# Kernel optimization log

Hardware: AMD Instinct MI355X
Metric: run time of the kernel (lower is better)

## Reference

```python
import jax, jax.numpy as jnp
import numpy as np

# ---- straight-through binary quantizers (custom VJP matches torch autograd.Functions) ----
@jax.custom_vjp
def bq(x):
    return jnp.sign(x)
def _bq_fwd(x):
    return jnp.sign(x), x
def _bq_bwd(x, g):
    return (g * ((x > -1.0) & (x < 1.0)).astype(g.dtype),)
bq.defvjp(_bq_fwd, _bq_bwd)

@jax.custom_vjp
def bq_quad(x):
    return jnp.sign(x)
def _bqq_fwd(x):
    return jnp.sign(x), x
def _bqq_bwd(x, g):
    return (jnp.maximum(2.0 - jnp.abs(2.0 * x), 0.0) * g,)
bq_quad.defvjp(_bqq_fwd, _bqq_bwd)

def bilinear(x, W, s, b):
    # BiLinear: row-centered sign weights scaled by learned per-row factor, sign activations
    Wc = W - jnp.mean(W, axis=-1, keepdims=True)
    Wb = s * bq(Wc)                      # (out, in)
    return bq(x) @ Wb.T + b

def selective_scan(u, delta, A, Bs, Cs, D, delta_bias):
    # u, delta: (B,K,Dn,L); A: (K,Dn,N); Bs,Cs: (B,K,N,L); D, delta_bias: (K,Dn)
    Bn, K, Dn, L = u.shape
    N = A.shape[-1]
    delta = jax.nn.softplus(delta + delta_bias[None, :, :, None])
    def step(h, inp):
        ut, dt, Bt, Ct = inp             # (B,K,Dn),(B,K,Dn),(B,K,N),(B,K,N)
        dA = jnp.exp(dt[..., None] * A[None])
        h = dA * h + (dt * ut)[..., None] * Bt[:, :, None, :]
        y = jnp.einsum('bkdn,bkn->bkd', h, Ct)
        return h, y
    h0 = jnp.zeros((Bn, K, Dn, N), u.dtype)
    _, ys = jax.lax.scan(step, h0,
                         (u.transpose(3, 0, 1, 2), delta.transpose(3, 0, 1, 2),
                          Bs.transpose(3, 0, 1, 2), Cs.transpose(3, 0, 1, 2)))
    y = ys.transpose(1, 2, 3, 0)         # (B,K,Dn,L)
    return y + D[None, :, :, None] * u

def _forward(x, W_in, b_in, s_in, move0_b, conv_W, conv_b, rp_b0, prelu_a, rp_b1,
             Wl, bl, sl, Wd, bd, sd, dt_bias, A_logs, Ds, ln_w, ln_b, W_out, b_out, s_out):
    Bn, H, Wi, dm = x.shape
    Dn = conv_W.shape[0]
    K = 4
    N = A_logs.shape[1]
    R = Wd.shape[2]
    L = H * Wi
    xz = bilinear(x, W_in, s_in, b_in)                  # (B,H,W,2*Dn)
    xp, z = jnp.split(xz, 2, axis=-1)
    xc = xp.transpose(0, 3, 1, 2)                       # (B,Dn,H,W)
    # BConv2d: move0 bias -> sign (quad STE) -> binary conv -> RPReLU -> residual
    t = bq_quad(xc + move0_b[None, :, None, None])
    sc = jax.lax.stop_gradient(jnp.mean(jnp.abs(conv_W), axis=(1, 2, 3), keepdims=True))
    cw = jnp.clip(conv_W, -1.0, 1.0)
    Wb = jax.lax.stop_gradient(sc * jnp.sign(conv_W) - cw) + cw
    t = jax.lax.conv_general_dilated(t, Wb, (1, 1), [(1, 1), (1, 1)],
                                     dimension_numbers=('NCHW', 'OIHW', 'NCHW'))
    t = t + conv_b[None, :, None, None]
    t = t + rp_b0[None, :, None, None]
    t = jnp.where(t >= 0, t, prelu_a[None, :, None, None] * t)
    t = t + rp_b1[None, :, None, None] + xc
    xconv = jax.nn.silu(t)
    # 4-direction scan inputs
    x_flat = xconv.reshape(Bn, Dn, L)
    x_tr = xconv.transpose(0, 1, 3, 2).reshape(Bn, Dn, L)
    x_hwwh = jnp.stack([x_flat, x_tr], axis=1)
    xs = jnp.concatenate([x_hwwh, jnp.flip(x_hwwh, axis=-1)], axis=1)   # (B,K,Dn,L)
    # NOTE: torch does .view(B,L,-1) on contiguous (B,Dn,L) slices = raw reshape (not transpose)
    xin = xs.reshape(Bn, K, L, Dn)
    x_dbl = jax.vmap(bilinear, in_axes=(1, 0, 0, 0), out_axes=1)(xin, Wl, sl, bl)  # (B,K,L,R+2N)
    x_dbl = x_dbl.transpose(0, 1, 3, 2)                                 # (B,K,R+2N,L)
    dts_r, Bs, Cs = jnp.split(x_dbl, [R, R + N], axis=2)
    dts_in = dts_r.reshape(Bn, K, L, R)  # raw reshape, matches torch .view
    dts = jax.vmap(bilinear, in_axes=(1, 0, 0, 0), out_axes=1)(dts_in, Wd, sd, bd)  # (B,K,L,Dn)
    dts = dts.transpose(0, 1, 3, 2)                                     # (B,K,Dn,L)
    A = -jnp.exp(A_logs).reshape(K, Dn, N)
    out_y = selective_scan(xs, dts, A, Bs, Cs, Ds.reshape(K, Dn), dt_bias.reshape(K, Dn))
    inv_y = jnp.flip(out_y[:, 2:4], axis=-1)
    wh_y = out_y[:, 1].reshape(Bn, Dn, Wi, H).transpose(0, 1, 3, 2).reshape(Bn, Dn, L)
    invwh_y = inv_y[:, 1].reshape(Bn, Dn, Wi, H).transpose(0, 1, 3, 2).reshape(Bn, Dn, L)
    y = out_y[:, 0] + inv_y[:, 0] + wh_y + invwh_y                      # (B,Dn,L)
    y = y.transpose(0, 2, 1).reshape(Bn, H, Wi, Dn)
    mu = jnp.mean(y, axis=-1, keepdims=True)
    var = jnp.var(y, axis=-1, keepdims=True)
    y = (y - mu) / jnp.sqrt(var + 1e-5) * ln_w + ln_b                   # LayerNorm eps=1e-5
    y = y * jax.nn.silu(z)
    return bilinear(y, W_out, s_out, b_out)

def setup_inputs():
    key = jax.random.key(0)
    ks = jax.random.split(key, 12)
    B, H, Wi, dm = 4, 64, 64, 96
    Dn, N, R, K = 192, 16, 6, 4
    u = lambda k, sh, a: jax.random.uniform(k, sh, jnp.float32, -a, a)
    x = jax.random.normal(ks[0], (B, H, Wi, dm), jnp.float32)
    W_in = u(ks[1], (2 * Dn, dm), 0.015)
    b_in = u(ks[2], (2 * Dn,), 0.01)
    s_in = jnp.mean(jnp.abs(W_in), axis=1, keepdims=True)
    move0_b = jnp.zeros((Dn,), jnp.float32)
    conv_W = 0.05 * jax.random.normal(ks[3], (Dn, Dn, 3, 3), jnp.float32)
    conv_b = u(ks[4], (Dn,), 0.01)
    rp_b0 = jnp.zeros((Dn,), jnp.float32)
    prelu_a = 0.25 * jnp.ones((Dn,), jnp.float32)
    rp_b1 = jnp.zeros((Dn,), jnp.float32)
    Wl = u(ks[5], (K, R + 2 * N, Dn), 0.015)
    bl = u(ks[6], (K, R + 2 * N), 0.01)
    sl = jnp.mean(jnp.abs(Wl), axis=2, keepdims=True)
    std = R ** -0.5
    Wd = u(ks[7], (K, Dn, R), std)
    bd = u(ks[8], (K, Dn), 0.01)
    sd = jnp.mean(jnp.abs(Wd), axis=2, keepdims=True)
    dt = jnp.exp(jax.random.uniform(ks[9], (K * Dn,), jnp.float32)
                 * (np.log(0.1) - np.log(0.001)) + np.log(0.001))
    dt = jnp.clip(dt, 1e-4, None)
    dt_bias = dt + jnp.log(-jnp.expm1(-dt))
    A_logs = jnp.tile(jnp.log(jnp.arange(1, N + 1, dtype=jnp.float32))[None, :], (K * Dn, 1))
    Ds = jnp.ones((K * Dn,), jnp.float32)
    ln_w = jnp.ones((Dn,), jnp.float32)
    ln_b = jnp.zeros((Dn,), jnp.float32)
    W_out = u(ks[10], (dm, Dn), 0.015)
    b_out = u(ks[11], (dm,), 0.01)
    s_out = jnp.mean(jnp.abs(W_out), axis=1, keepdims=True)
    return dict(x=x, W_in=W_in, b_in=b_in, s_in=s_in, move0_b=move0_b, conv_W=conv_W,
                conv_b=conv_b, rp_b0=rp_b0, prelu_a=prelu_a, rp_b1=rp_b1, Wl=Wl, bl=bl,
                sl=sl, Wd=Wd, bd=bd, sd=sd, dt_bias=dt_bias, A_logs=A_logs, Ds=Ds,
                ln_w=ln_w, ln_b=ln_b, W_out=W_out, b_out=b_out, s_out=s_out)

def reference(x, W_in, b_in, s_in, move0_b, conv_W, conv_b, rp_b0, prelu_a, rp_b1,
              Wl, bl, sl, Wd, bd, sd, dt_bias, A_logs, Ds, ln_w, ln_b, W_out, b_out, s_out):
    return _forward(x, W_in, b_in, s_in, move0_b, conv_W, conv_b, rp_b0, prelu_a, rp_b1,
                    Wl, bl, sl, Wd, bd, sd, dt_bias, A_logs, Ds, ln_w, ln_b, W_out, b_out, s_out)
```

## Files before the change

### kernel.cpp

```cpp
#include <hip/hip_runtime.h>
#include <math.h>
#include <stdint.h>

#define BB 4
#define HH 64
#define WW2 64
#define DM 96
#define DN 192
#define KK 4
#define NN 16
#define RR 6
#define LL 4096
#define RN 38

#define LOG2E 1.4426950408889634f
#define LN2   0.6931471805599453f

#define OFF_WDB      0
#define OFF_WCS      4608
#define OFF_WAUX     15360
#define OFF_WSC      16896
#define OFF_WBIB     17088
#define OFF_WOUTB    18240
#define OFF_WLBB     18816
#define OFF_XBP      19728
#define OFF_PXS      19728
#define OFF_SSUM     19728
#define OFF_YB       19728
#define OFF_XC       412992
#define OFF_ZS       3558720
#define OFF_XCONV    6704448
#define OFF_XS       9850176
#define OFF_XDBL     22433088
#define OFF_HEND     OFF_XCONV

#define PLANE 4356

__device__ __forceinline__ float fsign(float v) {
  return (v > 0.f) ? 1.f : ((v < 0.f) ? -1.f : 0.f);
}
__device__ __forceinline__ float softplusf(float v) {
  return fmaxf(v, 0.f) + LN2 * log2f(1.f + exp2f(-fabsf(v) * LOG2E));
}
__device__ __forceinline__ float siluf(float v) {
  return v / (1.f + expf(-v));
}
__device__ __forceinline__ float waveAllSum(float s) {
  #pragma unroll
  for (int off = 32; off; off >>= 1) s += __shfl_xor(s, off, 64);
  return s;
}

__global__ __launch_bounds__(64) void k_prep(
    const float* __restrict__ W_in, const float* __restrict__ s_in,
    const float* __restrict__ W_out, const float* __restrict__ s_out,
    const float* __restrict__ Wl, const float* __restrict__ sl,
    const float* __restrict__ Wd, const float* __restrict__ sd,
    const float* __restrict__ convW, float* __restrict__ ws) {
  int r = blockIdx.x, lane = threadIdx.x;
  if (r < 384) {
    const float* row = W_in + r * DM;
    float s = 0.f;
    for (int c = lane; c < DM; c += 64) s += row[c];
    s = waveAllSum(s);
    float mean = s / (float)DM;
    if (lane < 3) {
      uint32_t wv = 0;
      #pragma unroll
      for (int i = 0; i < 32; ++i) wv |= (row[lane * 32 + i] - mean > 0.f ? 1u : 0u) << i;
      ((uint32_t*)(ws + OFF_WBIB))[r * 3 + lane] = wv;
    }
  } else if (r < 480) {
    int m = r - 384;
    const float* row = W_out + m * DN;
    float s = 0.f;
    for (int c = lane; c < DN; c += 64) s += row[c];
    s = waveAllSum(s);
    float mean = s / (float)DN;
    if (lane < 6) {
      uint32_t wv = 0;
      #pragma unroll
      for (int i = 0; i < 32; ++i) wv |= (row[lane * 32 + i] - mean > 0.f ? 1u : 0u) << i;
      ((uint32_t*)(ws + OFF_WOUTB))[m * 6 + lane] = wv;
    }
  } else if (r < 632) {
    int idx = r - 480;
    const float* row = Wl + idx * DN;
    float s = 0.f;
    for (int c = lane; c < DN; c += 64) s += row[c];
    s = waveAllSum(s);
    float mean = s / (float)DN;
    if (lane < 6) {
      uint32_t wv = 0;
      #pragma unroll
      for (int i = 0; i < 32; ++i) wv |= (row[lane * 32 + i] - mean > 0.f ? 1u : 0u) << i;
      ((uint32_t*)(ws + OFF_WLBB))[idx * 6 + lane] = wv;
    }
  } else if (r < 1400) {
    int idx = r - 632;
    const float* row = Wd + idx * RR;
    float s = (lane < RR) ? row[lane] : 0.f;
    s = waveAllSum(s);
    float mean = s / (float)RR;
    unsigned long long mb = __ballot((lane < RR) && (row[lane] - mean > 0.f));
    if (lane == 0) {
      ((uint32_t*)(ws + OFF_WDB))[idx] = (uint32_t)mb & 0x3Fu;
      (ws + OFF_WDB)[768 + idx] = sd[idx];
    }
  } else {
    int o = r - 1400;
    const float* row = convW + o * 1728;
    float s = 0.f;
    for (int j = lane; j < 1728; j += 64) s += fabsf(row[j]);
    s = waveAllSum(s);
    float sc = s / 1728.f;
    uint32_t* wb = (uint32_t*)(ws + OFF_WCS);
    int* aux = (int*)(ws + OFF_WAUX);
    float* scf = ws + OFF_WSC;
    uint32_t word = 0;
    if (lane < 54) {
      int cw = lane / 9, tap = lane % 9;
      #pragma unroll
      for (int i = 0; i < 32; ++i)
        word |= (row[(cw * 32 + i) * 9 + tap] > 0.f ? 1u : 0u) << i;
      wb[o * 56 + lane] = word;
    } else if (lane < 56) {
      wb[o * 56 + lane] = 0u;
    }
    int pc = (lane < 54) ? 2 * (int)__popc(word) - 32 : 0;
    int tapid = lane % 9;
    int wst = 0;
    #pragma unroll
    for (int cw = 0; cw < 6; ++cw) wst += __shfl(pc, cw * 9 + tapid, 64);
    int w_t[9];
    #pragma unroll
    for (int t9 = 0; t9 < 9; ++t9) w_t[t9] = __shfl(wst, t9, 64);
    if (lane == 0) {
      aux[o * 8 + 0] = w_t[0] + w_t[3] + w_t[6];
      aux[o * 8 + 1] = w_t[2] + w_t[5] + w_t[8];
      aux[o * 8 + 2] = w_t[0] + w_t[1] + w_t[2];
      aux[o * 8 + 3] = w_t[6] + w_t[7] + w_t[8];
      aux[o * 8 + 4] = w_t[0];
      aux[o * 8 + 5] = w_t[2];
      aux[o * 8 + 6] = w_t[6];
      aux[o * 8 + 7] = w_t[8];
      scf[o] = sc;
    }
  }
}

__global__ __launch_bounds__(384) void k_bilin_in(
    const float* __restrict__ x, const float* __restrict__ b_in,
    const float* __restrict__ s_in, const float* __restrict__ ws,
    float* __restrict__ xc, float* __restrict__ zs) {
  __shared__ uint32_t spx[16 * 3];
  __shared__ float sxz[384 * 17];
  int p0 = blockIdx.x * 16;
  if (threadIdx.x < 48) {
    int pix = threadIdx.x / 3, wd = threadIdx.x % 3;
    const float* base = x + (size_t)(p0 + pix) * DM + wd * 32;
    uint32_t wv = 0;
    #pragma unroll
    for (int i = 0; i < 32; ++i) wv |= (base[i] > 0.f ? 1u : 0u) << i;
    spx[pix * 3 + wd] = wv;
  }
  __syncthreads();
  int o = threadIdx.x;
  uint32_t w0, w1, w2;
  {
    const uint32_t* wb = (const uint32_t*)(ws + OFF_WBIB) + o * 3;
    w0 = wb[0]; w1 = wb[1]; w2 = wb[2];
  }
  float bias = b_in[o], sc = s_in[o];
  #pragma unroll
  for (int pix = 0; pix < 16; ++pix) {
    int P = (int)__popc(spx[pix * 3 + 0] ^ w0) + (int)__popc(spx[pix * 3 + 1] ^ w1) +
            (int)__popc(spx[pix * 3 + 2] ^ w2);
    sxz[o * 17 + pix] = bias + sc * (float)(DM - 2 * P);
  }
  __syncthreads();
  int b = p0 >> 12, l0 = p0 & 4095;
  for (int f = threadIdx.x; f < DN * 16; f += 384) {
    int od = f >> 4, pix = f & 15;
    xc[((size_t)(b * DN + od)) * LL + l0 + pix] = sxz[od * 17 + pix];
  }
  for (int f = threadIdx.x; f < DN * 16; f += 384) {
    int pix = f / DN, oz = f - pix * DN;
    zs[(size_t)(p0 + pix) * DN + oz] = siluf(sxz[(DN + oz) * 17 + pix]);
  }
}

__global__ __launch_bounds__(256) void k_pack(
    const float* __restrict__ xc, const float* __restrict__ move0,
    uint32_t* __restrict__ xb) {
  int t = blockIdx.x * 256 + threadIdx.x;
  int w2 = t & 31;
  int h = (t >> 5) & 63;
  int g = t >> 11;
  int cw = g % 6, b = g / 6;
  const float* xp = xc + ((size_t)(b * DN + cw * 32)) * LL + h * 64 + w2 * 2;
  uint32_t w0 = 0, w1 = 0;
  #pragma unroll
  for (int i = 0; i < 32; ++i) {
    float m = move0[cw * 32 + i];
    float2 v = *(const float2*)(xp + (size_t)i * LL);
    w0 |= (v.x + m > 0.f ? 1u : 0u) << i;
    w1 |= (v.y + m > 0.f ? 1u : 0u) << i;
  }
  uint32_t* plane = xb + (size_t)(b * 6 + cw) * PLANE;
  plane[(h + 1) * 66 + 1 + w2 * 2] = w0;
  plane[(h + 1) * 66 + 2 + w2 * 2] = w1;
}

__global__ __launch_bounds__(256) void k_conv(
    const uint32_t* __restrict__ xb, const float* __restrict__ xc,
    const uint32_t* __restrict__ wbits, const int* __restrict__ aux,
    const float* __restrict__ scf, const float* __restrict__ conv_b,
    const float* __restrict__ rp_b0, const float* __restrict__ prelu_a,
    const float* __restrict__ rp_b1, float* __restrict__ xconv) {
  int og = blockIdx.x & 3;
  int stripe = (blockIdx.x >> 2) & 15;
  int b = blockIdx.x >> 6;
  int w = threadIdx.x & 63, r = threadIdx.x >> 6;
  int h = stripe * 4 + r;

  __shared__ uint32_t swb[48 * 56];
  __shared__ int saux[48 * 8];
  __shared__ float sconst[48 * 4];
  for (int i = threadIdx.x; i < 48 * 56; i += 256) swb[i] = wbits[og * (48 * 56) + i];
  for (int i = threadIdx.x; i < 48 * 8; i += 256) saux[i] = aux[og * (48 * 8) + i];
  if (threadIdx.x < 48) {
    int o = og * 48 + threadIdx.x;
    sconst[threadIdx.x * 4 + 0] = scf[o];
    sconst[threadIdx.x * 4 + 1] = conv_b[o] + rp_b0[o];
    sconst[threadIdx.x * 4 + 2] = prelu_a[o];
    sconst[threadIdx.x * 4 + 3] = rp_b1[o];
  }

  uint32_t xw[6][9];
  const uint32_t* xpb = xb + (size_t)b * 6 * PLANE;
  #pragma unroll
  for (int cw = 0; cw < 6; ++cw) {
    const uint32_t* plane = xpb + cw * PLANE + (h + 1) * 66 + (w + 1);
    #pragma unroll
    for (int dy = 0; dy < 3; ++dy) {
      #pragma unroll
      for (int dx = 0; dx < 3; ++dx)
        xw[cw][dy * 3 + dx] = plane[(dy - 1) * 66 + (dx - 1)];
    }
  }
  bool isL = (w == 0), isR = (w == 63);
  bool isT = (h == 0), isB = (h == 63);
  const float* xcp = xc + ((size_t)(b * DN + og * 48)) * LL + h * 64 + w;
  float* xop = xconv + ((size_t)(b * DN + og * 48)) * LL + h * 64 + w;
  __syncthreads();

  #pragma unroll 1
  for (int oc = 0; oc < 48; ++oc) {
    const uint32_t* wp = &swb[oc * 56];
    int P = 0;
    #pragma unroll
    for (int cw = 0; cw < 6; ++cw) {
      int pp = 0;
      #pragma unroll
      for (int t = 0; t < 9; ++t) pp += (int)__popc(wp[cw * 9 + t] ^ xw[cw][t]);
      P += pp;
    }
    int corr = isL ? saux[oc * 8 + 0] : (isR ? saux[oc * 8 + 1] : 0);
    if (isT) {
      corr += saux[oc * 8 + 2];
      if (isL) corr -= saux[oc * 8 + 4];
      if (isR) corr -= saux[oc * 8 + 5];
    }
    if (isB) {
      corr += saux[oc * 8 + 3];
      if (isL) corr -= saux[oc * 8 + 6];
      if (isR) corr -= saux[oc * 8 + 7];
    }
    float acc = sconst[oc * 4 + 0] * (float)(1728 - 2 * P + corr);
    float t = acc + sconst[oc * 4 + 1];
    t = (t >= 0.f) ? t : sconst[oc * 4 + 2] * t;
    t += sconst[oc * 4 + 3] + *xcp;
    *xop = siluf(t);
    xcp += LL; xop += LL;
  }
}

__global__ __launch_bounds__(256) void k_build_xs(const float* __restrict__ xconv,
                                                  float* __restrict__ xs,
                                                  uint32_t* __restrict__ pxs) {
  __shared__ float tile[64][65];
  int bd = blockIdx.x;
  int b = bd / DN, d = bd % DN;
  const float* img = xconv + (size_t)bd * LL;
  for (int i = threadIdx.x; i < LL; i += 256)
    tile[i >> 6][i & 63] = img[i];
  __syncthreads();
  int lane = threadIdx.x & 63;
  #pragma unroll
  for (int k = 0; k < 4; ++k) {
    size_t base = ((size_t)((b * KK + k) * DN + d)) * LL;
    for (int j = threadIdx.x; j < LL; j += 256) {
      float v;
      if (k == 0)      v = tile[j >> 6][j & 63];
      else if (k == 1) v = tile[j & 63][j >> 6];
      else if (k == 2) { int t2 = 4095 - j; v = tile[t2 >> 6][t2 & 63]; }
      else             { int t2 = 4095 - j; v = tile[t2 & 63][t2 >> 6]; }
      xs[base + j] = v;
      unsigned long long m = __ballot(v > 0.f);
      if (lane == 0)       pxs[(base + j) >> 5] = (uint32_t)m;
      else if (lane == 32) pxs[(base + j) >> 5] = (uint32_t)(m >> 32);
    }
  }
}

__global__ __launch_bounds__(256) void k_xdbl(
    const uint32_t* __restrict__ pxs, const float* __restrict__ ws,
    const float* __restrict__ bl, const float* __restrict__ sl,
    float* __restrict__ xdbl) {
  int bk = blockIdx.x >> 4;
  int l = ((blockIdx.x & 15) << 8) + threadIdx.x;
  int k = bk & 3;
  __shared__ uint32_t swl[RN * 6];
  __shared__ float sbias[RN], ssc[RN];
  if (threadIdx.x < RN * 6) swl[threadIdx.x] = ((const uint32_t*)(ws + OFF_WLBB))[k * RN * 6 + threadIdx.x];
  if (threadIdx.x < RN) {
    sbias[threadIdx.x] = bl[k * RN + threadIdx.x];
    ssc[threadIdx.x] = sl[k * RN + threadIdx.x];
  }
  uint32_t xb[6];
  const uint32_t* pp = pxs + (size_t)bk * 24576 + (size_t)l * 6;
  #pragma unroll
  for (int j = 0; j < 6; ++j) xb[j] = pp[j];
  __syncthreads();
  float* xo = xdbl + (size_t)bk * (RN * LL) + l;
  #pragma unroll 1
  for (int o = 0; o < RN; ++o) {
    int P = 0;
    #pragma unroll
    for (int j = 0; j < 6; ++j) P += (int)__popc(xb[j] ^ swl[o * 6 + j]);
    xo[(size_t)o * LL] = sbias[o] + ssc[o] * (float)(DN - 2 * P);
  }
}

__device__ __forceinline__ void rpowers(float r, float* a) {
  float r2 = r * r, r3 = r2 * r, r4 = r2 * r2, r8 = r4 * r4;
  a[0] = r;       a[1] = r2;      a[2] = r3;      a[3] = r4;
  a[4] = r4 * r;  a[5] = r4 * r2; a[6] = r4 * r3; a[7] = r8;
  a[8] = r8 * r;  a[9] = r8 * r2; a[10] = r8 * r3; a[11] = r8 * r4;
  a[12] = r8 * a[4]; a[13] = r8 * a[5]; a[14] = r8 * a[6]; a[15] = r8 * r8;
}

__global__ __launch_bounds__(192) void k_scan_a(
    const float* __restrict__ xs, const float* __restrict__ xdbl,
    const float* __restrict__ ws, const float* __restrict__ bd,
    const float* __restrict__ dt_bias, const float* __restrict__ A_logs,
    float* __restrict__ hend, float* __restrict__ Ssum) {
  int c = blockIdx.x & 63;
  int bk = blockIdx.x >> 6;
  int k = bk & 3;
  int d = threadIdx.x;
  int t0 = c << 6;
  __shared__ uint32_t sdtm[64];
  __shared__ float4 sB4[256];
  float* sBf = (float*)sB4;
  const float* dtbase = xdbl + (size_t)bk * (RN * LL);
  if (d < 64) {
    const float2* p2 = (const float2*)(dtbase + t0 * 6 + d * 6);
    float2 a = p2[0], bb = p2[1], cc = p2[2];
    uint32_t m = (a.x > 0.f ? 1u : 0u) | (a.y > 0.f ? 2u : 0u) |
                 (bb.x > 0.f ? 4u : 0u) | (bb.y > 0.f ? 8u : 0u) |
                 (cc.x > 0.f ? 16u : 0u) | (cc.y > 0.f ? 32u : 0u);
    sdtm[d] = m;
  }
  {
    const float4* Bp = (const float4*)(xdbl + ((size_t)bk * RN + RR) * LL);
    for (int i = d; i < 256; i += 192) {
      int n = i >> 4, j = i & 15;
      float4 v = Bp[n * 1024 + (t0 >> 2) + j];
      sBf[(4 * j + 0) * 16 + n] = v.x;
      sBf[(4 * j + 1) * 16 + n] = v.y;
      sBf[(4 * j + 2) * 16 + n] = v.z;
      sBf[(4 * j + 3) * 16 + n] = v.w;
    }
  }
  uint32_t w6 = ((const uint32_t*)(ws + OFF_WDB))[k * DN + d];
  float sdv = (ws + OFF_WDB)[768 + k * DN + d];
  float biasd = bd[k * DN + d] + dt_bias[k * DN + d];
  float Araw[16];
  bool fok = true;
  {
    const float* ap = A_logs + (k * DN + d) * NN;
    #pragma unroll
    for (int n = 0; n < NN; ++n) {
      Araw[n] = -expf(ap[n]);
      fok = fok && (fabsf(Araw[n] + (float)(n + 1)) < 1e-3f);
    }
  }
  bool fastpath = (__ballot(fok) == ~0ull);
  float h[16];
  #pragma unroll
  for (int n = 0; n < NN; ++n) h[n] = 0.f;
  float S = 0.f;
  const float* up = xs + ((size_t)bk * DN + d) * LL + t0;
  __syncthreads();
  if (fastpath) {
    #pragma unroll 1
    for (int tt = 0; tt < 16; ++tt) {
      float4 u4 = *(const float4*)(up + 4 * tt);
      #pragma unroll
      for (int q = 0; q < 4; ++q) {
        int t = 4 * tt + q;
        float uv = (q == 0) ? u4.x : (q == 1) ? u4.y : (q == 2) ? u4.z : u4.w;
        int pc = (int)__popc(sdtm[t] ^ w6);
        float dv = softplusf(biasd + sdv * (float)(RR - 2 * pc));
        float rr = exp2f(-dv * LOG2E);
        S += dv;
        float du = dv * uv;
        float a[16];
        rpowers(rr, a);
        #pragma unroll
        for (int g = 0; g < 4; ++g) {
          float4 bv = sB4[t * 4 + g];
          h[4 * g + 0] = a[4 * g + 0] * h[4 * g + 0] + du * bv.x;
          h[4 * g + 1] = a[4 * g + 1] * h[4 * g + 1] + du * bv.y;
          h[4 * g + 2] = a[4 * g + 2] * h[4 * g + 2] + du * bv.z;
          h[4 * g + 3] = a[4 * g + 3] * h[4 * g + 3] + du * bv.w;
        }
      }
    }
  } else {
    float An[16];
    #pragma unroll
    for (int n = 0; n < NN; ++n) An[n] = Araw[n] * LOG2E;
    #pragma unroll 1
    for (int tt = 0; tt < 16; ++tt) {
      float4 u4 = *(const float4*)(up + 4 * tt);
      #pragma unroll
      for (int q = 0; q < 4; ++q) {
        int t = 4 * tt + q;
        float uv = (q == 0) ? u4.x : (q == 1) ? u4.y : (q == 2) ? u4.z : u4.w;
        int pc = (int)__popc(sdtm[t] ^ w6);
        float dv = softplusf(biasd + sdv * (float)(RR - 2 * pc));
        S += dv;
        float du = dv * uv;
        #pragma unroll
        for (int g = 0; g < 4; ++g) {
          float4 bv = sB4[t * 4 + g];
          float a0 = exp2f(dv * An[4 * g + 0]);
          float a1 = exp2f(dv * An[4 * g + 1]);
          float a2 = exp2f(dv * An[4 * g + 2]);
          float a3 = exp2f(dv * An[4 * g + 3]);
          h[4 * g + 0] = a0 * h[4 * g + 0] + du * bv.x;
          h[4 * g + 1] = a1 * h[4 * g + 1] + du * bv.y;
          h[4 * g + 2] = a2 * h[4 * g + 2] + du * bv.z;
          h[4 * g + 3] = a3 * h[4 * g + 3] + du * bv.w;
        }
      }
    }
  }
  float* hp = hend + (size_t)c * 49152 + (size_t)(bk * DN + d) * 16;
  #pragma unroll
  for (int n = 0; n < NN; n += 4)
    *(float4*)(hp + n) = make_float4(h[n], h[n + 1], h[n + 2], h[n + 3]);
  Ssum[c * 3072 + bk * DN + d] = S;
}

__global__ __launch_bounds__(256) void k_scan_b(
    const float* __restrict__ A_logs, const float* __restrict__ Ssum,
    float* __restrict__ hend) {
  int tid = blockIdx.x * 256 + threadIdx.x;
  int bkd = tid >> 4, n = tid & 15;
  int bk = bkd / DN, d = bkd - bk * DN;
  int k = bk & 3;
  float An2 = -expf(A_logs[(k * DN + d) * NN + n]) * LOG2E;
  float h = 0.f;
  float Sc = Ssum[bkd];
  float he = hend[tid];
  #pragma unroll 1
  for (int c = 0; c < 64; ++c) {
    float Sn = 0.f, hn = 0.f;
    if (c < 63) {
      Sn = Ssum[(c + 1) * 3072 + bkd];
      hn = hend[(size_t)(c + 1) * 49152 + tid];
    }
    hend[(size_t)c * 49152 + tid] = h;
    h = exp2f(An2 * Sc) * h + he;
    Sc = Sn; he = hn;
  }
}

__global__ __launch_bounds__(192) void k_scan_c(
    const float* __restrict__ xs, const float* __restrict__ xdbl,
    const float* __restrict__ ws, const float* __restrict__ bd,
    const float* __restrict__ dt_bias, const float* __restrict__ A_logs,
    const float* __restrict__ Ds, const float* __restrict__ h0buf,
    float* __restrict__ y) {
  int c = blockIdx.x & 63;
  int bk = blockIdx.x >> 6;
  int k = bk & 3;
  int d = threadIdx.x;
  int t0 = c << 6;
  __shared__ uint32_t sdtm[64];
  __shared__ float4 sB4[256];
  __shared__ float4 sC4[256];
  float* sBf = (float*)sB4;
  float* sCf = (float*)sC4;
  const float* dtbase = xdbl + (size_t)bk * (RN * LL);
  if (d < 64) {
    const float2* p2 = (const float2*)(dtbase + t0 * 6 + d * 6);
    float2 a = p2[0], bb = p2[1], cc = p2[2];
    uint32_t m = (a.x > 0.f ? 1u : 0u) | (a.y > 0.f ? 2u : 0u) |
                 (bb.x > 0.f ? 4u : 0u) | (bb.y > 0.f ? 8u : 0u) |
                 (cc.x > 0.f ? 16u : 0u) | (cc.y > 0.f ? 32u : 0u);
    sdtm[d] = m;
  }
  {
    const float4* Bp = (const float4*)(xdbl + ((size_t)bk * RN + RR) * LL);
    const float4* Cp = (const float4*)(xdbl + ((size_t)bk * RN + RR + NN) * LL);
    for (int i = d; i < 256; i += 192) {
      int n = i >> 4, j = i & 15;
      float4 v = Bp[n * 1024 + (t0 >> 2) + j];
      sBf[(4 * j + 0) * 16 + n] = v.x;
      sBf[(4 * j + 1) * 16 + n] = v.y;
      sBf[(4 * j + 2) * 16 + n] = v.z;
      sBf[(4 * j + 3) * 16 + n] = v.w;
      float4 w = Cp[n * 1024 + (t0 >> 2) + j];
      sCf[(4 * j + 0) * 16 + n] = w.x;
      sCf[(4 * j + 1) * 16 + n] = w.y;
      sCf[(4 * j + 2) * 16 + n] = w.z;
      sCf[(4 * j + 3) * 16 + n] = w.w;
    }
  }
  uint32_t w6 = ((const uint32_t*)(ws + OFF_WDB))[k * DN + d];
  float sdv = (ws + OFF_WDB)[768 + k * DN + d];
  float biasd = bd[k * DN + d] + dt_bias[k * DN + d];
  float Dd = Ds[k * DN + d];
  float Araw[16];
  bool fok = true;
  {
    const float* ap = A_logs + (k * DN + d) * NN;
    #pragma unroll
    for (int n = 0; n < NN; ++n) {
      Araw[n] = -expf(ap[n]);
      fok = fok && (fabsf(Araw[n] + (float)(n + 1)) < 1e-3f);
    }
  }
  bool fastpath = (__ballot(fok) == ~0ull);
  float h[16];
  {
    const float* hp = h0buf + (size_t)c * 49152 + (size_t)(bk * DN + d) * 16;
    #pragma unroll
    for (int n = 0; n < NN; n += 4) {
      float4 v = *(const float4*)(hp + n);
      h[n] = v.x; h[n + 1] = v.y; h[n + 2] = v.z; h[n + 3] = v.w;
    }
  }
  const float* up = xs + ((size_t)bk * DN + d) * LL + t0;
  float* yb = y + (size_t)(bk >> 2) * (LL * DN);
  __syncthreads();
  if (fastpath) {
    #pragma unroll 1
    for (int tt = 0; tt < 16; ++tt) {
      float4 u4 = *(const float4*)(up + 4 * tt);
      #pragma unroll
      for (int q = 0; q < 4; ++q) {
        int t = 4 * tt + q;
        float uv = (q == 0) ? u4.x : (q == 1) ? u4.y : (q == 2) ? u4.z : u4.w;
        int pc = (int)__popc(sdtm[t] ^ w6);
        float dv = softplusf(biasd + sdv * (float)(RR - 2 * pc));
        float rr = exp2f(-dv * LOG2E);
        float du = dv * uv;
        float yv = Dd * uv;
        float a[16];
        rpowers(rr, a);
        #pragma unroll
        for (int g = 0; g < 4; ++g) {
          float4 bv = sB4[t * 4 + g];
          float4 cv = sC4[t * 4 + g];
          h[4 * g + 0] = a[4 * g + 0] * h[4 * g + 0] + du * bv.x;
          h[4 * g + 1] = a[4 * g + 1] * h[4 * g + 1] + du * bv.y;
          h[4 * g + 2] = a[4 * g + 2] * h[4 * g + 2] + du * bv.z;
          h[4 * g + 3] = a[4 * g + 3] * h[4 * g + 3] + du * bv.w;
          yv += cv.x * h[4 * g + 0];
          yv += cv.y * h[4 * g + 1];
          yv += cv.z * h[4 * g + 2];
          yv += cv.w * h[4 * g + 3];
        }
        int ta = t0 + t, l;
        if (k == 0)      l = ta;
        else if (k == 1) l = ((ta & 63) << 6) | (ta >> 6);
        else if (k == 2) l = 4095 - ta;
        else { int t2 = 4095 - ta; l = ((t2 & 63) << 6) | (t2 >> 6); }
        atomicAdd(&yb[(size_t)l * DN + d], yv);
      }
    }
  } else {
    float An[16];
    #pragma unroll
    for (int n = 0; n < NN; ++n) An[n] = Araw[n] * LOG2E;
    #pragma unroll 1
    for (int tt = 0; tt < 16; ++tt) {
      float4 u4 = *(const float4*)(up + 4 * tt);
      #pragma unroll
      for (int q = 0; q < 4; ++q) {
        int t = 4 * tt + q;
        float uv = (q == 0) ? u4.x : (q == 1) ? u4.y : (q == 2) ? u4.z : u4.w;
        int pc = (int)__popc(sdtm[t] ^ w6);
        float dv = softplusf(biasd + sdv * (float)(RR - 2 * pc));
        float du = dv * uv;
        float yv = Dd * uv;
        #pragma unroll
        for (int g = 0; g < 4; ++g) {
          float4 bv = sB4[t * 4 + g];
          float4 cv = sC4[t * 4 + g];
          float a0 = exp2f(dv * An[4 * g + 0]);
          float a1 = exp2f(dv * An[4 * g + 1]);
          float a2 = exp2f(dv * An[4 * g + 2]);
          float a3 = exp2f(dv * An[4 * g + 3]);
          h[4 * g + 0] = a0 * h[4 * g + 0] + du * bv.x;
          h[4 * g + 1] = a1 * h[4 * g + 1] + du * bv.y;
          h[4 * g + 2] = a2 * h[4 * g + 2] + du * bv.z;
          h[4 * g + 3] = a3 * h[4 * g + 3] + du * bv.w;
          yv += cv.x * h[4 * g + 0];
          yv += cv.y * h[4 * g + 1];
          yv += cv.z * h[4 * g + 2];
          yv += cv.w * h[4 * g + 3];
        }
        int ta = t0 + t, l;
        if (k == 0)      l = ta;
        else if (k == 1) l = ((ta & 63) << 6) | (ta >> 6);
        else if (k == 2) l = 4095 - ta;
        else { int t2 = 4095 - ta; l = ((t2 & 63) << 6) | (t2 >> 6); }
        atomicAdd(&yb[(size_t)l * DN + d], yv);
      }
    }
  }
}

__global__ __launch_bounds__(256) void k_ln(
    const float* __restrict__ y, const float* __restrict__ zs,
    const float* __restrict__ ln_w, const float* __restrict__ ln_b,
    uint32_t* __restrict__ ybits) {
  __shared__ float ty[64 * 193];
  __shared__ float ps[256];
  __shared__ float smu[64], srs[64];
  __shared__ float slw[DN], slb[DN];
  int b = blockIdx.x >> 6;
  int l0 = (blockIdx.x & 63) << 6;
  const float* yp = y + (size_t)(b * LL + l0) * DN;
  if (threadIdx.x < DN) {
    slw[threadIdx.x] = ln_w[threadIdx.x];
    slb[threadIdx.x] = ln_b[threadIdx.x];
  }
  {
    int lc = threadIdx.x / DN, d2 = threadIdx.x - lc * DN;
    for (int i = threadIdx.x; i < 64 * DN; i += 256) {
      ty[lc * 193 + d2] = yp[i];
      d2 += 256;
      if (d2 >= DN) { d2 -= DN; lc += 1; if (d2 >= DN) { d2 -= DN; lc += 1; } }
    }
  }
  __syncthreads();
  int lc = threadIdx.x & 63, part = threadIdx.x >> 6;
  float s = 0.f;
  for (int d = part * 48; d < part * 48 + 48; ++d) s += ty[lc * 193 + d];
  ps[threadIdx.x] = s;
  __syncthreads();
  if (threadIdx.x < 64)
    smu[threadIdx.x] = (ps[threadIdx.x] + ps[threadIdx.x + 64] +
                        ps[threadIdx.x + 128] + ps[threadIdx.x + 192]) / (float)DN;
  __syncthreads();
  float mu = smu[lc];
  float q = 0.f;
  for (int d = part * 48; d < part * 48 + 48; ++d) {
    float v = ty[lc * 193 + d] - mu; q += v * v;
  }
  ps[threadIdx.x] = q;
  __syncthreads();
  if (threadIdx.x < 64) {
    float var = (ps[threadIdx.x] + ps[threadIdx.x + 64] +
                 ps[threadIdx.x + 128] + ps[threadIdx.x + 192]) / (float)DN;
    srs[threadIdx.x] = rsqrtf(var + 1e-5f);
  }
  __syncthreads();
  for (int item = threadIdx.x; item < 64 * 6; item += 256) {
    int lc2 = item / 6, wd = item % 6;
    float mu2 = smu[lc2], rs2 = srs[lc2];
    const float* zb = zs + (size_t)(b * LL + l0 + lc2) * DN + wd * 32;
    uint32_t wv = 0;
    #pragma unroll
    for (int i = 0; i < 32; ++i) {
      int d = wd * 32 + i;
      float ln = (ty[lc2 * 193 + d] - mu2) * rs2 * slw[d] + slb[d];
      wv |= ((ln * zb[i] > 0.f) ? 1u : 0u) << i;
    }
    ybits[(size_t)(b * LL + l0 + lc2) * 6 + wd] = wv;
  }
}

__global__ __launch_bounds__(256) void k_out(
    const uint32_t* __restrict__ ybits, const float* __restrict__ ws,
    const float* __restrict__ b_out, const float* __restrict__ s_out,
    float* __restrict__ out) {
  __shared__ uint32_t sy[64 * 6];
  __shared__ uint32_t swo[96 * 6];
  __shared__ float sb[96], ssc[96];
  int p0 = blockIdx.x * 64;
  for (int i = threadIdx.x; i < 64 * 6; i += 256) sy[i] = ybits[(size_t)p0 * 6 + i];
  for (int i = threadIdx.x; i < 96 * 6; i += 256) swo[i] = ((const uint32_t*)(ws + OFF_WOUTB))[i];
  if (threadIdx.x < 96) {
    sb[threadIdx.x] = b_out[threadIdx.x];
    ssc[threadIdx.x] = s_out[threadIdx.x];
  }
  __syncthreads();
  for (int oi = threadIdx.x; oi < 64 * DM; oi += 256) {
    int pr = oi / DM, m = oi % DM;
    int P = 0;
    #pragma unroll
    for (int j = 0; j < 6; ++j) P += (int)__popc(sy[pr * 6 + j] ^ swo[m * 6 + j]);
    out[(size_t)(p0 + pr) * DM + m] = sb[m] + ssc[m] * (float)(DN - 2 * P);
  }
}

extern "C" void kernel_launch(void* const* d_in, const int* in_sizes, int n_in,
                              void* d_out, int out_size, void* d_ws, size_t ws_size,
                              hipStream_t stream) {
  const float* x       = (const float*)d_in[0];
  const float* W_in    = (const float*)d_in[1];
  const float* b_in    = (const float*)d_in[2];
  const float* s_in    = (const float*)d_in[3];
  const float* move0_b = (const float*)d_in[4];
  const float* conv_W  = (const float*)d_in[5];
  const float* conv_b  = (const float*)d_in[6];
  const float* rp_b0   = (const float*)d_in[7];
  const float* prelu_a = (const float*)d_in[8];
  const float* rp_b1   = (const float*)d_in[9];
  const float* Wl      = (const float*)d_in[10];
  const float* bl      = (const float*)d_in[11];
  const float* sl      = (const float*)d_in[12];
  const float* Wd      = (const float*)d_in[13];
  const float* bd      = (const float*)d_in[14];
  const float* sd      = (const float*)d_in[15];
  const float* dt_bias = (const float*)d_in[16];
  const float* A_logs  = (const float*)d_in[17];
  const float* Ds      = (const float*)d_in[18];
  const float* ln_w    = (const float*)d_in[19];
  const float* ln_b    = (const float*)d_in[20];
  const float* W_out   = (const float*)d_in[21];
  const float* b_out   = (const float*)d_in[22];
  const float* s_out   = (const float*)d_in[23];
  float* ws  = (float*)d_ws;
  float* out = (float*)d_out;

  hipLaunchKernelGGL(k_prep, dim3(1592), dim3(64), 0, stream,
                     W_in, s_in, W_out, s_out, Wl, sl, Wd, sd, conv_W, ws);
  hipLaunchKernelGGL(k_bilin_in, dim3(1024), dim3(384), 0, stream,
                     x, b_in, s_in, ws, ws + OFF_XC, ws + OFF_ZS);
  hipMemsetAsync((void*)(ws + OFF_XBP), 0, (size_t)(4 * 6 * PLANE) * 4, stream);
  hipLaunchKernelGGL(k_pack, dim3(192), dim3(256), 0, stream,
                     ws + OFF_XC, move0_b, (uint32_t*)(ws + OFF_XBP));
  hipLaunchKernelGGL(k_conv, dim3(256), dim3(256), 0, stream,
                     (const uint32_t*)(ws + OFF_XBP), ws + OFF_XC,
                     (const uint32_t*)(ws + OFF_WCS), (const int*)(ws + OFF_WAUX),
                     ws + OFF_WSC, conv_b, rp_b0, prelu_a, rp_b1,
                     ws + OFF_XCONV);
  hipLaunchKernelGGL(k_build_xs, dim3(768), dim3(256), 0, stream,
                     ws + OFF_XCONV, ws + OFF_XS, (uint32_t*)(ws + OFF_PXS));
  hipLaunchKernelGGL(k_xdbl, dim3(256), dim3(256), 0, stream,
                     (const uint32_t*)(ws + OFF_PXS), ws, bl, sl, ws + OFF_XDBL);
  hipLaunchKernelGGL(k_scan_a, dim3(1024), dim3(192), 0, stream,
                     ws + OFF_XS, ws + OFF_XDBL, ws, bd, dt_bias, A_logs,
                     ws + OFF_HEND, ws + OFF_SSUM);
  hipLaunchKernelGGL(k_scan_b, dim3(192), dim3(256), 0, stream,
                     A_logs, ws + OFF_SSUM, ws + OFF_HEND);
  hipMemsetAsync((void*)(ws + OFF_XC), 0, (size_t)3145728 * sizeof(float), stream);
  hipLaunchKernelGGL(k_scan_c, dim3(1024), dim3(192), 0, stream,
                     ws + OFF_XS, ws + OFF_XDBL, ws, bd, dt_bias, A_logs, Ds,
                     ws + OFF_HEND, ws + OFF_XC);
  hipLaunchKernelGGL(k_ln, dim3(256), dim3(256), 0, stream,
                     ws + OFF_XC, ws + OFF_ZS, ln_w, ln_b, (uint32_t*)(ws + OFF_YB));
  hipLaunchKernelGGL(k_out, dim3(256), dim3(256), 0, stream,
                     (const uint32_t*)(ws + OFF_YB), ws, b_out, s_out, out);
}
```

Before: 341.8 us.

## Fuse bit-packing into input bilinear and tabulate softplus per popcount in scans

The separate k_pack kernel is removed. k_bilin_in now packs the sign bits of xc+move0 straight from its shared-memory tile into the padded bit planes, which saves one launch and a re-read of xc from global memory. In both scan kernels, dt can only take seven values per channel (popcount 0..6), so softplus and exp(-dt) are precomputed once into shared-memory tables instead of being evaluated every timestep. k_prep also stages each conv weight row in shared memory before the strided bit gather; this adds shared memory and a barrier in exchange for fewer strided global reads.

Measured after the change: 327.1 us. 1.04x faster.

```diff
diff --git a/kernel.cpp b/kernel.cpp
--- a/kernel.cpp
+++ b/kernel.cpp
@@ -57,6 +57,7 @@
     const float* __restrict__ Wl, const float* __restrict__ sl,
     const float* __restrict__ Wd, const float* __restrict__ sd,
     const float* __restrict__ convW, float* __restrict__ ws) {
+  __shared__ float srow[1728];
   int r = blockIdx.x, lane = threadIdx.x;
   if (r < 384) {
     const float* row = W_in + r * DM;
@@ -111,8 +112,13 @@
     int o = r - 1400;
     const float* row = convW + o * 1728;
     float s = 0.f;
-    for (int j = lane; j < 1728; j += 64) s += fabsf(row[j]);
+    for (int j = lane; j < 1728; j += 64) {
+      float v = row[j];
+      srow[j] = v;
+      s += fabsf(v);
+    }
     s = waveAllSum(s);
+    __syncthreads();
     float sc = s / 1728.f;
     uint32_t* wb = (uint32_t*)(ws + OFF_WCS);
     int* aux = (int*)(ws + OFF_WAUX);
@@ -122,7 +128,7 @@
       int cw = lane / 9, tap = lane % 9;
       #pragma unroll
       for (int i = 0; i < 32; ++i)
-        word |= (row[(cw * 32 + i) * 9 + tap] > 0.f ? 1u : 0u) << i;
+        word |= (srow[(cw * 32 + i) * 9 + tap] > 0.f ? 1u : 0u) << i;
       wb[o * 56 + lane] = word;
     } else if (lane < 56) {
       wb[o * 56 + lane] = 0u;
@@ -151,10 +157,12 @@
 
 __global__ __launch_bounds__(384) void k_bilin_in(
     const float* __restrict__ x, const float* __restrict__ b_in,
-    const float* __restrict__ s_in, const float* __restrict__ ws,
-    float* __restrict__ xc, float* __restrict__ zs) {
+    const float* __restrict__ s_in, const float* __restrict__ move0,
+    const float* __restrict__ ws, float* __restrict__ xc, float* __restrict__ zs,
+    uint32_t* __restrict__ xb) {
   __shared__ uint32_t spx[16 * 3];
   __shared__ float sxz[384 * 17];
+  __shared__ float smv[DN];
   int p0 = blockIdx.x * 16;
   if (threadIdx.x < 48) {
     int pix = threadIdx.x / 3, wd = threadIdx.x % 3;
@@ -164,6 +172,7 @@
     for (int i = 0; i < 32; ++i) wv |= (base[i] > 0.f ? 1u : 0u) << i;
     spx[pix * 3 + wd] = wv;
   }
+  if (threadIdx.x < DN) smv[threadIdx.x] = move0[threadIdx.x];
   __syncthreads();
   int o = threadIdx.x;
   uint32_t w0, w1, w2;
@@ -188,28 +197,18 @@
     int pix = f / DN, oz = f - pix * DN;
     zs[(size_t)(p0 + pix) * DN + oz] = siluf(sxz[(DN + oz) * 17 + pix]);
   }
-}
-
-__global__ __launch_bounds__(256) void k_pack(
-    const float* __restrict__ xc, const float* __restrict__ move0,
-    uint32_t* __restrict__ xb) {
-  int t = blockIdx.x * 256 + threadIdx.x;
-  int w2 = t & 31;
-  int h = (t >> 5) & 63;
-  int g = t >> 11;
-  int cw = g % 6, b = g / 6;
-  const float* xp = xc + ((size_t)(b * DN + cw * 32)) * LL + h * 64 + w2 * 2;
-  uint32_t w0 = 0, w1 = 0;
-  #pragma unroll
-  for (int i = 0; i < 32; ++i) {
-    float m = move0[cw * 32 + i];
-    float2 v = *(const float2*)(xp + (size_t)i * LL);
-    w0 |= (v.x + m > 0.f ? 1u : 0u) << i;
-    w1 |= (v.y + m > 0.f ? 1u : 0u) << i;
-  }
-  uint32_t* plane = xb + (size_t)(b * 6 + cw) * PLANE;
-  plane[(h + 1) * 66 + 1 + w2 * 2] = w0;
-  plane[(h + 1) * 66 + 2 + w2 * 2] = w1;
+  if (threadIdx.x < 96) {
+    int pix = threadIdx.x / 6, cw = threadIdx.x % 6;
+    uint32_t wv = 0;
+    #pragma unroll
+    for (int i = 0; i < 32; ++i) {
+      int dch = cw * 32 + i;
+      wv |= ((sxz[dch * 17 + pix] + smv[dch] > 0.f) ? 1u : 0u) << i;
+    }
+    int l = l0 + pix, h = l >> 6, w = l & 63;
+    uint32_t* plane = xb + (size_t)(b * 6 + cw) * PLANE;
+    plane[(h + 1) * 66 + 1 + w] = wv;
+  }
 }
 
 __global__ __launch_bounds__(256) void k_conv(
@@ -363,6 +362,7 @@
   int t0 = c << 6;
   __shared__ uint32_t sdtm[64];
   __shared__ float4 sB4[256];
+  __shared__ float sDV[7 * 192], sR[7 * 192];
   float* sBf = (float*)sB4;
   const float* dtbase = xdbl + (size_t)bk * (RN * LL);
   if (d < 64) {
@@ -387,6 +387,12 @@
   uint32_t w6 = ((const uint32_t*)(ws + OFF_WDB))[k * DN + d];
   float sdv = (ws + OFF_WDB)[768 + k * DN + d];
   float biasd = bd[k * DN + d] + dt_bias[k * DN + d];
+  #pragma unroll
+  for (int pc = 0; pc < 7; ++pc) {
+    float dv = softplusf(biasd + sdv * (float)(RR - 2 * pc));
+    sDV[pc * 192 + d] = dv;
+    sR[pc * 192 + d] = exp2f(-dv * LOG2E);
+  }
   float Araw[16];
   bool fok = true;
   {
@@ -413,8 +419,8 @@
         int t = 4 * tt + q;
         float uv = (q == 0) ? u4.x : (q == 1) ? u4.y : (q == 2) ? u4.z : u4.w;
         int pc = (int)__popc(sdtm[t] ^ w6);
-        float dv = softplusf(biasd + sdv * (float)(RR - 2 * pc));
-        float rr = exp2f(-dv * LOG2E);
+        float dv = sDV[pc * 192 + d];
+        float rr = sR[pc * 192 + d];
         S += dv;
         float du = dv * uv;
         float a[16];
@@ -441,7 +447,7 @@
         int t = 4 * tt + q;
         float uv = (q == 0) ? u4.x : (q == 1) ? u4.y : (q == 2) ? u4.z : u4.w;
         int pc = (int)__popc(sdtm[t] ^ w6);
-        float dv = softplusf(biasd + sdv * (float)(RR - 2 * pc));
+        float dv = sDV[pc * 192 + d];
         S += dv;
         float du = dv * uv;
         #pragma unroll
@@ -504,6 +510,7 @@
   __shared__ uint32_t sdtm[64];
   __shared__ float4 sB4[256];
   __shared__ float4 sC4[256];
+  __shared__ float sDV[7 * 192], sR[7 * 192];
   float* sBf = (float*)sB4;
   float* sCf = (float*)sC4;
   const float* dtbase = xdbl + (size_t)bk * (RN * LL);
@@ -536,6 +543,12 @@
   float sdv = (ws + OFF_WDB)[768 + k * DN + d];
   float biasd = bd[k * DN + d] + dt_bias[k * DN + d];
   float Dd = Ds[k * DN + d];
+  #pragma unroll
+  for (int pc = 0; pc < 7; ++pc) {
+    float dv = softplusf(biasd + sdv * (float)(RR - 2 * pc));
+    sDV[pc * 192 + d] = dv;
+    sR[pc * 192 + d] = exp2f(-dv * LOG2E);
+  }
   float Araw[16];
   bool fok = true;
   {
@@ -568,8 +581,8 @@
         int t = 4 * tt + q;
         float uv = (q == 0) ? u4.x : (q == 1) ? u4.y : (q == 2) ? u4.z : u4.w;
         int pc = (int)__popc(sdtm[t] ^ w6);
-        float dv = softplusf(biasd + sdv * (float)(RR - 2 * pc));
-        float rr = exp2f(-dv * LOG2E);
+        float dv = sDV[pc * 192 + d];
+        float rr = sR[pc * 192 + d];
         float du = dv * uv;
         float yv = Dd * uv;
         float a[16];
@@ -607,7 +620,7 @@
         int t = 4 * tt + q;
         float uv = (q == 0) ? u4.x : (q == 1) ? u4.y : (q == 2) ? u4.z : u4.w;
         int pc = (int)__popc(sdtm[t] ^ w6);
-        float dv = softplusf(biasd + sdv * (float)(RR - 2 * pc));
+        float dv = sDV[pc * 192 + d];
         float du = dv * uv;
         float yv = Dd * uv;
         #pragma unroll
@@ -755,11 +768,10 @@
 
   hipLaunchKernelGGL(k_prep, dim3(1592), dim3(64), 0, stream,
                      W_in, s_in, W_out, s_out, Wl, sl, Wd, sd, conv_W, ws);
+  hipMemsetAsync((void*)(ws + OFF_XBP), 0, (size_t)(4 * 6 * PLANE) * 4, stream);
   hipLaunchKernelGGL(k_bilin_in, dim3(1024), dim3(384), 0, stream,
-                     x, b_in, s_in, ws, ws + OFF_XC, ws + OFF_ZS);
-  hipMemsetAsync((void*)(ws + OFF_XBP), 0, (size_t)(4 * 6 * PLANE) * 4, stream);
-  hipLaunchKernelGGL(k_pack, dim3(192), dim3(256), 0, stream,
-                     ws + OFF_XC, move0_b, (uint32_t*)(ws + OFF_XBP));
+                     x, b_in, s_in, move0_b, ws, ws + OFF_XC, ws + OFF_ZS,
+                     (uint32_t*)(ws + OFF_XBP));
   hipLaunchKernelGGL(k_conv, dim3(256), dim3(256), 0, stream,
                      (const uint32_t*)(ws + OFF_XBP), ws + OFF_XC,
                      (const uint32_t*)(ws + OFF_WCS), (const int*)(ws + OFF_WAUX),
```
